# Performance work log

Hardware: AMD Instinct MI355X
Metric: run time of the kernel (lower is better)

## Reference

```python
import jax, jax.numpy as jnp
import numpy as np

B, S, D, H, F, NL, V = 4, 2048, 512, 8, 2048, 4, 32000
DH = D // H
EPS = 1e-6
LN_EPS = 1e-5


def _xavier(k, shape):
    lim = (6.0 / (shape[-2] + shape[-1])) ** 0.5
    return jax.random.uniform(k, shape, jnp.float32, -lim, lim)


def setup_inputs() -> dict:
    key = jax.random.key(0)
    ks = jax.random.split(key, 12)
    x = jax.random.randint(ks[0], (B, S), 0, V)
    emb = jax.random.normal(ks[1], (V, D), jnp.float32) * 0.02
    # sinusoidal positional encoding
    pos = np.arange(S, dtype=np.float32)[:, None]
    div = np.exp(np.arange(0, D, 2, dtype=np.float32) * (-np.log(10000.0) / D))
    pe_np = np.zeros((S, D), np.float32)
    pe_np[:, 0::2] = np.sin(pos * div)
    pe_np[:, 1::2] = np.cos(pos * div)
    pe = jnp.asarray(pe_np)
    return {
        "x": x, "emb": emb, "pe": pe,
        "Wq": _xavier(ks[2], (NL, D, D)), "bq": jnp.zeros((NL, D)),
        "Wk": _xavier(ks[3], (NL, D, D)), "bk": jnp.zeros((NL, D)),
        "Wv": _xavier(ks[4], (NL, D, D)), "bv": jnp.zeros((NL, D)),
        "Wo": _xavier(ks[5], (NL, D, D)), "bo": jnp.zeros((NL, D)),
        "W1": _xavier(ks[6], (NL, D, F)), "b1": jnp.zeros((NL, F)),
        "W2": _xavier(ks[7], (NL, F, D)), "b2": jnp.zeros((NL, D)),
        "g1": jnp.ones((NL, D)), "be1": jnp.zeros((NL, D)),
        "g2": jnp.ones((NL, D)), "be2": jnp.zeros((NL, D)),
        "gf": jnp.ones((D,)), "bf": jnp.zeros((D,)),
    }


def _layer_norm(h, g, b):
    mu = jnp.mean(h, axis=-1, keepdims=True)
    var = jnp.mean((h - mu) ** 2, axis=-1, keepdims=True)
    return (h - mu) * jax.lax.rsqrt(var + LN_EPS) * g + b


def _phi(u):
    # elu(x) + 1 feature map of fast-transformers causal-linear attention
    return jax.nn.elu(u) + 1.0


def _causal_linear_attention(q, k, v, key_mask):
    # q, k, v: [B, S, H, DH]; key_mask: [B, S] (1 for valid keys)
    Q = _phi(q)
    K = _phi(k) * key_mask[:, :, None, None]
    # cumulative state sum_{j<=i} K_j outer V_j : [B, S, H, DH, DH]
    St = jnp.cumsum(K[..., :, None] * v[..., None, :], axis=1)
    num = jnp.einsum("bshd,bshde->bshe", Q, St)
    Z = 1.0 / (jnp.einsum("bshd,bshd->bsh", Q, jnp.cumsum(K, axis=1)) + EPS)
    return num * Z[..., None]


def reference(x, emb, pe, Wq, bq, Wk, bk, Wv, bv, Wo, bo,
              W1, b1, W2, b2, g1, be1, g2, be2, gf, bf):
    # length mask from nonzero token count (LengthMask semantics)
    lengths = jnp.sum(jnp.abs(x) != 0, axis=-1)  # [B]
    key_mask = (jnp.arange(S)[None, :] < lengths[:, None]).astype(jnp.float32)
    h = emb[x] + pe[None, :, :]  # [B, S, D]
    for i in range(NL):
        q = (h @ Wq[i] + bq[i]).reshape(B, S, H, DH)
        k = (h @ Wk[i] + bk[i]).reshape(B, S, H, DH)
        v = (h @ Wv[i] + bv[i]).reshape(B, S, H, DH)
        a = _causal_linear_attention(q, k, v, key_mask).reshape(B, S, D)
        a = a @ Wo[i] + bo[i]
        h = _layer_norm(h + a, g1[i], be1[i])
        y = jax.nn.relu(h @ W1[i] + b1[i]) @ W2[i] + b2[i]
        h = _layer_norm(h + y, g2[i], be2[i])
    return _layer_norm(h, gf, bf)
```

## Files before the change

kernel.cpp:

```cpp
#include <hip/hip_runtime.h>
#include <math.h>

#define NLAYER 4
#define BB 4
#define SS 2048
#define DD 512
#define HH 8
#define DH 64
#define FF 2048
#define TT (BB*SS)
#define LCH 64
#define NCH (SS/LCH)
#define LN_EPS 1e-5f
#define ATT_EPS 1e-6f

typedef __bf16 bf16x8 __attribute__((ext_vector_type(8)));
typedef float  f32x4  __attribute__((ext_vector_type(4)));

__device__ __forceinline__ unsigned short f2bf(float f) {
    union { float f; unsigned u; } a; a.f = f;
    unsigned u = a.u;
    unsigned r = (u + 0x7FFFu + ((u >> 16) & 1u)) >> 16;
    return (unsigned short)r;
}
__device__ __forceinline__ float bf2f(unsigned short s) {
    union { unsigned u; float f; } a; a.u = ((unsigned)s) << 16;
    return a.f;
}
__device__ __forceinline__ float phi_f(float u) {
    return u > 0.f ? u + 1.f : __expf(u);
}

__global__ __launch_bounds__(64)
void len_kernel(const int* __restrict__ x, int* __restrict__ len) {
    const int b = blockIdx.x;
    int cnt = 0;
    for (int s = threadIdx.x; s < SS; s += 64) cnt += (x[b * SS + s] != 0);
    #pragma unroll
    for (int off = 32; off; off >>= 1) cnt += __shfl_xor(cnt, off);
    if (threadIdx.x == 0) len[b] = cnt;
}

__global__ __launch_bounds__(256)
void embed_kernel(const int* __restrict__ x, const float* __restrict__ emb,
                  const float* __restrict__ pe, float* __restrict__ h,
                  unsigned short* __restrict__ h_bf) {
    int t = blockIdx.x * 256 + threadIdx.x;
    int row = t >> 7;
    int q = t & 127;
    int tok = x[row];
    int s = row & (SS - 1);
    float4 e = ((const float4*)(emb + (size_t)tok * DD))[q];
    float4 p = ((const float4*)(pe + (size_t)s * DD))[q];
    float4 v; v.x = e.x + p.x; v.y = e.y + p.y; v.z = e.z + p.z; v.w = e.w + p.w;
    ((float4*)(h + (size_t)row * DD))[q] = v;
    ushort4 ub; ub.x = f2bf(v.x); ub.y = f2bf(v.y); ub.z = f2bf(v.z); ub.w = f2bf(v.w);
    ((ushort4*)(h_bf + (size_t)row * DD))[q] = ub;
}

__global__ __launch_bounds__(256)
void transpose_cvt(const float* __restrict__ src, unsigned short* __restrict__ dst,
                   int R, int C, size_t srcLS, size_t dstLS) {
    __shared__ float tile[32][33];
    const int z = blockIdx.z;
    src += (size_t)z * srcLS;
    dst += (size_t)z * dstLS;
    const int c0 = blockIdx.x * 32, r0 = blockIdx.y * 32;
    const int tx = threadIdx.x & 31, ty = threadIdx.x >> 5;
    #pragma unroll
    for (int i = 0; i < 32; i += 8)
        tile[ty + i][tx] = src[(size_t)(r0 + ty + i) * C + c0 + tx];
    __syncthreads();
    #pragma unroll
    for (int i = 0; i < 32; i += 8)
        dst[(size_t)(c0 + ty + i) * R + r0 + tx] = f2bf(tile[tx][ty + i]);
}

__global__ __launch_bounds__(256)
void bias_concat(const float* __restrict__ bq, const float* __restrict__ bk,
                 const float* __restrict__ bv, float* __restrict__ bqkv) {
    int idx = blockIdx.x * 256 + threadIdx.x;
    if (idx >= NLAYER * 1536) return;
    int l = idx / 1536, n = idx % 1536;
    float v = n < 512 ? bq[l * 512 + n] : (n < 1024 ? bk[l * 512 + n - 512] : bv[l * 512 + n - 1024]);
    bqkv[idx] = v;
}

__device__ __forceinline__ void gll16(void* lds_ptr, const void* g_ptr) {
    __builtin_amdgcn_global_load_lds(
        (const __attribute__((address_space(1))) void*)g_ptr,
        (__attribute__((address_space(3))) void*)lds_ptr, 16, 0, 0);
}

template<int RELU, int WF, int WB>
__global__ __launch_bounds__(256, 2)
void gemm_bt(const unsigned short* __restrict__ A, const unsigned short* __restrict__ Bt,
             const float* __restrict__ bias, float* __restrict__ Cf,
             unsigned short* __restrict__ Cb, int M, int N, int K) {
    __shared__ __align__(16) char lds[2 * 2 * 128 * 64 * 2];
    const int m0 = blockIdx.x * 128;
    const int n0 = blockIdx.y * 128;
    const int tid = threadIdx.x;
    const int w = tid >> 6, lane = tid & 63;
    const int wr = w >> 1, wc = w & 1;
    const int srow = lane >> 3, scc = lane & 7;

    f32x4 acc[4][4] = {};

    auto stage = [&](int buf, int k0) {
        char* base = lds + buf * 32768;
        #pragma unroll
        for (int op = 0; op < 2; ++op) {
            const unsigned short* G = op ? Bt : A;
            const int r0 = op ? n0 : m0;
            char* obase = base + op * 16384;
            #pragma unroll
            for (int i = 0; i < 4; ++i) {
                int ii = w * 4 + i;
                int row = ii * 8 + srow;
                int chunk = scc ^ (row & 7);
                gll16(obase + ii * 1024,
                      G + (size_t)(r0 + row) * K + k0 + chunk * 8);
            }
        }
    };

    stage(0, 0);
    const int nt = K >> 6;
    int buf = 0;
    const int g = lane >> 4;
    const int rA = wr * 64 + (lane & 15);
    const int rB = wc * 64 + (lane & 15);

    for (int kt = 0; kt < nt; ++kt) {
        __syncthreads();
        if (kt + 1 < nt) stage(buf ^ 1, (kt + 1) << 6);
        const char* pA = lds + buf * 32768;
        const char* pB = pA + 16384;
        bf16x8 af[4][2], bfr[4][2];
        #pragma unroll
        for (int m = 0; m < 4; ++m)
            #pragma unroll
            for (int kk = 0; kk < 2; ++kk) {
                int row = rA + m * 16;
                int c = (kk * 4 + g) ^ (row & 7);
                af[m][kk] = *(const bf16x8*)(pA + row * 128 + c * 16);
            }
        #pragma unroll
        for (int n = 0; n < 4; ++n)
            #pragma unroll
            for (int kk = 0; kk < 2; ++kk) {
                int row = rB + n * 16;
                int c = (kk * 4 + g) ^ (row & 7);
                bfr[n][kk] = *(const bf16x8*)(pB + row * 128 + c * 16);
            }
        #pragma unroll
        for (int kk = 0; kk < 2; ++kk)
            #pragma unroll
            for (int m = 0; m < 4; ++m)
                #pragma unroll
                for (int n = 0; n < 4; ++n)
                    acc[m][n] = __builtin_amdgcn_mfma_f32_16x16x32_bf16(
                        af[m][kk], bfr[n][kk], acc[m][n], 0, 0, 0);
        buf ^= 1;
    }

    const int col16 = lane & 15;
    const int rgrp = lane >> 4;
    #pragma unroll
    for (int n = 0; n < 4; ++n) {
        int col = n0 + wc * 64 + n * 16 + col16;
        float bi = bias[col];
        #pragma unroll
        for (int m = 0; m < 4; ++m) {
            int rowb = m0 + wr * 64 + m * 16 + rgrp * 4;
            #pragma unroll
            for (int r = 0; r < 4; ++r) {
                float v = acc[m][n][r] + bi;
                if (RELU) v = v > 0.f ? v : 0.f;
                if (WF) Cf[(size_t)(rowb + r) * N + col] = v;
                if (WB) Cb[(size_t)(rowb + r) * N + col] = f2bf(v);
            }
        }
    }
}

__global__ __launch_bounds__(256)
void attn_chunk_sums(const float* __restrict__ qkv, const int* __restrict__ len,
                     float* __restrict__ states, float* __restrict__ ksum) {
    const int c = blockIdx.x & (NCH - 1);
    const int bh = blockIdx.x / NCH;
    const int b = bh >> 3, h = bh & 7;
    const int L = len[b];
    const int tid = threadIdx.x;
    const int w = tid >> 6, lane = tid & 63;
    __shared__ __align__(16) unsigned short Kt[64 * 64];
    __shared__ __align__(16) unsigned short Vt[64 * 64];
    __shared__ float ksumP[4][64];

    float kpart = 0.f;
    #pragma unroll 8
    for (int t = 0; t < 16; ++t) {
        const int jj = 4 * t + w;
        const int d = lane;
        const int sglob = c * 64 + jj;
        const float* base = qkv + (size_t)(b * SS + sglob) * 1536 + h * 64 + d;
        float kv = base[512], vv = base[1024];
        float kp = (sglob < L) ? phi_f(kv) : 0.f;
        kpart += kp;
        const int sw = (((jj >> 3) ^ (d & 7)) << 3) + (jj & 7);
        Kt[d * 64 + sw] = f2bf(kp);
        Vt[d * 64 + sw] = f2bf(vv);
    }
    ksumP[w][lane] = kpart;
    __syncthreads();

    const int frow = w * 16 + (lane & 15);
    const int g = lane >> 4;
    bf16x8 ak[2];
    #pragma unroll
    for (int kk = 0; kk < 2; ++kk)
        ak[kk] = *(const bf16x8*)&Kt[frow * 64 + (((kk * 4 + g) ^ (frow & 7)) << 3)];
    f32x4 oc[4] = {};
    #pragma unroll
    for (int ef = 0; ef < 4; ++ef) {
        int brow = ef * 16 + (lane & 15);
        #pragma unroll
        for (int kk = 0; kk < 2; ++kk) {
            bf16x8 bv = *(const bf16x8*)&Vt[brow * 64 + (((kk * 4 + g) ^ (brow & 7)) << 3)];
            oc[ef] = __builtin_amdgcn_mfma_f32_16x16x32_bf16(ak[kk], bv, oc[ef], 0, 0, 0);
        }
    }
    float* so = states + (size_t)blockIdx.x * 4096;
    #pragma unroll
    for (int ef = 0; ef < 4; ++ef)
        #pragma unroll
        for (int r = 0; r < 4; ++r) {
            int dd = w * 16 + g * 4 + r;
            int e = ef * 16 + (lane & 15);
            so[dd * 64 + e] = oc[ef][r];
        }
    if (w == 0) {
        float s = ksumP[0][lane] + ksumP[1][lane] + ksumP[2][lane] + ksumP[3][lane];
        ksum[(size_t)blockIdx.x * 64 + lane] = s;
    }
}

__global__ __launch_bounds__(256)
void attn_prefix(const float* __restrict__ states, const float* __restrict__ ksum,
                 float* __restrict__ sprefix, float* __restrict__ kprefix) {
    const int bh = blockIdx.x >> 4;
    const int idx = (blockIdx.x & 15) * 256 + threadIdx.x;
    size_t base = (size_t)bh * NCH * 4096 + idx;
    float run = 0.f;
    #pragma unroll 4
    for (int cc = 0; cc < NCH; ++cc) {
        size_t o = base + (size_t)cc * 4096;
        float v = states[o];
        sprefix[o] = run;
        run += v;
    }
    if ((blockIdx.x & 15) == 0 && threadIdx.x < 64) {
        size_t kb = (size_t)bh * NCH * 64 + threadIdx.x;
        float krun = 0.f;
        for (int cc = 0; cc < NCH; ++cc) {
            size_t o = kb + (size_t)cc * 64;
            float v = ksum[o];
            kprefix[o] = krun;
            krun += v;
        }
    }
}

__global__ __launch_bounds__(256)
void attn_output(const float* __restrict__ qkv, const int* __restrict__ len,
                 const float* __restrict__ sprefix, const float* __restrict__ kprefix,
                 unsigned short* __restrict__ a_bf) {
    const int c = blockIdx.x & (NCH - 1);
    const int bh = blockIdx.x / NCH;
    const int b = bh >> 3, h = bh & 7;
    const int L = len[b];
    const int tid = threadIdx.x;
    const int w = tid >> 6, lane = tid & 63;

    __shared__ __align__(16) unsigned short Qb[64 * 64];
    __shared__ __align__(16) unsigned short Kb[64 * 64];
    __shared__ __align__(16) unsigned short SpT[64 * 64];
    __shared__ __align__(16) unsigned short Vt[64 * 64];
    __shared__ __align__(16) unsigned short Amb[64 * 64];
    __shared__ float zq[64];
    __shared__ float zinv[64];

    const float kspv = kprefix[(size_t)(bh * NCH + c) * 64 + lane];
    const float* Sp = sprefix + (size_t)(bh * NCH + c) * 4096;

    #pragma unroll 4
    for (int t = 0; t < 16; ++t) {
        const int jj = 4 * t + w;
        const int d = lane;
        const int sglob = c * 64 + jj;
        const float* base = qkv + (size_t)(b * SS + sglob) * 1536 + h * 64 + d;
        float qv = base[0], kv = base[512], vv = base[1024];
        float qp = phi_f(qv);
        float kp = (sglob < L) ? phi_f(kv) : 0.f;
        const int swr = (((d >> 3) ^ (jj & 7)) << 3) + (d & 7);
        Qb[jj * 64 + swr] = f2bf(qp);
        Kb[jj * 64 + swr] = f2bf(kp);
        const int swt = (((jj >> 3) ^ (d & 7)) << 3) + (jj & 7);
        Vt[d * 64 + swt] = f2bf(vv);
        float spv = Sp[jj * 64 + d];
        SpT[d * 64 + swt] = f2bf(spv);
        float zc = qp * kspv;
        #pragma unroll
        for (int off = 32; off; off >>= 1) zc += __shfl_xor(zc, off);
        if (lane == 0) zq[jj] = zc;
    }
    __syncthreads();

    const int frow = w * 16 + (lane & 15);
    const int g = lane >> 4;
    bf16x8 aq[2];
    #pragma unroll
    for (int kk = 0; kk < 2; ++kk)
        aq[kk] = *(const bf16x8*)&Qb[frow * 64 + (((kk * 4 + g) ^ (frow & 7)) << 3)];

    f32x4 am[4] = {};
    #pragma unroll
    for (int jf = 0; jf < 4; ++jf) {
        int brow = jf * 16 + (lane & 15);
        #pragma unroll
        for (int kk = 0; kk < 2; ++kk) {
            bf16x8 bk = *(const bf16x8*)&Kb[brow * 64 + (((kk * 4 + g) ^ (brow & 7)) << 3)];
            am[jf] = __builtin_amdgcn_mfma_f32_16x16x32_bf16(aq[kk], bk, am[jf], 0, 0, 0);
        }
    }

    float zl[4] = {0.f, 0.f, 0.f, 0.f};
    #pragma unroll
    for (int jf = 0; jf < 4; ++jf) {
        #pragma unroll
        for (int r = 0; r < 4; ++r) {
            int i = w * 16 + g * 4 + r;
            int j = jf * 16 + (lane & 15);
            float v = (j <= i) ? am[jf][r] : 0.f;
            zl[r] += v;
            Amb[i * 64 + (((j >> 3) ^ (i & 7)) << 3) + (j & 7)] = f2bf(v);
        }
    }
    #pragma unroll
    for (int r = 0; r < 4; ++r)
        #pragma unroll
        for (int off = 1; off < 16; off <<= 1) zl[r] += __shfl_xor(zl[r], off);
    #pragma unroll
    for (int r = 0; r < 4; ++r) {
        if ((lane & 15) == r) {
            int i = w * 16 + g * 4 + r;
            zinv[i] = 1.f / (zl[r] + zq[i] + ATT_EPS);
        }
    }

    f32x4 oc[4] = {};
    #pragma unroll
    for (int ef = 0; ef < 4; ++ef) {
        int brow = ef * 16 + (lane & 15);
        #pragma unroll
        for (int kk = 0; kk < 2; ++kk) {
            bf16x8 bs = *(const bf16x8*)&SpT[brow * 64 + (((kk * 4 + g) ^ (brow & 7)) << 3)];
            oc[ef] = __builtin_amdgcn_mfma_f32_16x16x32_bf16(aq[kk], bs, oc[ef], 0, 0, 0);
        }
    }
    bf16x8 aam[2];
    #pragma unroll
    for (int kk = 0; kk < 2; ++kk)
        aam[kk] = *(const bf16x8*)&Amb[frow * 64 + (((kk * 4 + g) ^ (frow & 7)) << 3)];
    #pragma unroll
    for (int ef = 0; ef < 4; ++ef) {
        int brow = ef * 16 + (lane & 15);
        #pragma unroll
        for (int kk = 0; kk < 2; ++kk) {
            bf16x8 bv = *(const bf16x8*)&Vt[brow * 64 + (((kk * 4 + g) ^ (brow & 7)) << 3)];
            oc[ef] = __builtin_amdgcn_mfma_f32_16x16x32_bf16(aam[kk], bv, oc[ef], 0, 0, 0);
        }
    }

    __syncthreads();
    #pragma unroll
    for (int ef = 0; ef < 4; ++ef) {
        #pragma unroll
        for (int r = 0; r < 4; ++r) {
            int i = w * 16 + g * 4 + r;
            int e = ef * 16 + (lane & 15);
            float zi = zinv[i];
            Kb[i * 64 + (((e >> 3) ^ (i & 7)) << 3) + (e & 7)] = f2bf(oc[ef][r] * zi);
        }
    }
    __syncthreads();
    {
        unsigned short* dst = a_bf + (size_t)(b * SS + c * 64) * 512 + h * 64;
        #pragma unroll
        for (int u = 0; u < 2; ++u) {
            int cid = tid + u * 256;
            int row = cid >> 3, cb = cid & 7;
            int4 val = *(const int4*)&Kb[row * 64 + ((cb ^ (row & 7)) << 3)];
            *(int4*)(dst + (size_t)row * 512 + cb * 8) = val;
        }
    }
}

template<int ADD, int WB>
__global__ __launch_bounds__(64)
void ln_kernel(const float* __restrict__ hin, const float* __restrict__ add,
               const float* __restrict__ gw, const float* __restrict__ bw,
               float* __restrict__ hout, unsigned short* __restrict__ hbf) {
    const int row = blockIdx.x;
    const int lane = threadIdx.x;
    float v[8];
    const float* hp = hin + (size_t)row * DD;
    float s = 0.f;
    #pragma unroll
    for (int i = 0; i < 2; ++i) {
        int q = lane + i * 64;
        float4 a = ((const float4*)hp)[q];
        if (ADD) {
            float4 bb = ((const float4*)(add + (size_t)row * DD))[q];
            a.x += bb.x; a.y += bb.y; a.z += bb.z; a.w += bb.w;
        }
        v[i*4+0] = a.x; v[i*4+1] = a.y; v[i*4+2] = a.z; v[i*4+3] = a.w;
        s += a.x + a.y + a.z + a.w;
    }
    #pragma unroll
    for (int off = 32; off; off >>= 1) s += __shfl_xor(s, off);
    float mu = s * (1.f / 512.f);
    float sq = 0.f;
    #pragma unroll
    for (int i = 0; i < 8; ++i) { float d = v[i] - mu; sq += d * d; }
    #pragma unroll
    for (int off = 32; off; off >>= 1) sq += __shfl_xor(sq, off);
    float rs = 1.f / sqrtf(sq * (1.f / 512.f) + LN_EPS);
    #pragma unroll
    for (int i = 0; i < 2; ++i) {
        int q = lane + i * 64;
        float4 gv = ((const float4*)gw)[q];
        float4 bv = ((const float4*)bw)[q];
        float4 o;
        o.x = (v[i*4+0] - mu) * rs * gv.x + bv.x;
        o.y = (v[i*4+1] - mu) * rs * gv.y + bv.y;
        o.z = (v[i*4+2] - mu) * rs * gv.z + bv.z;
        o.w = (v[i*4+3] - mu) * rs * gv.w + bv.w;
        ((float4*)(hout + (size_t)row * DD))[q] = o;
        if (WB) {
            ushort4 ub; ub.x = f2bf(o.x); ub.y = f2bf(o.y); ub.z = f2bf(o.z); ub.w = f2bf(o.w);
            ((ushort4*)(hbf + (size_t)row * DD))[q] = ub;
        }
    }
}

extern "C" void kernel_launch(void* const* d_in, const int* in_sizes, int n_in,
                              void* d_out, int out_size, void* d_ws, size_t ws_size,
                              hipStream_t stream) {
    (void)in_sizes; (void)n_in; (void)out_size; (void)ws_size;
    const int*   x   = (const int*)d_in[0];
    const float* emb = (const float*)d_in[1];
    const float* pe  = (const float*)d_in[2];
    const float* Wq  = (const float*)d_in[3];
    const float* bq  = (const float*)d_in[4];
    const float* Wk  = (const float*)d_in[5];
    const float* bk  = (const float*)d_in[6];
    const float* Wv  = (const float*)d_in[7];
    const float* bv  = (const float*)d_in[8];
    const float* Wo  = (const float*)d_in[9];
    const float* bo  = (const float*)d_in[10];
    const float* W1  = (const float*)d_in[11];
    const float* b1  = (const float*)d_in[12];
    const float* W2  = (const float*)d_in[13];
    const float* b2  = (const float*)d_in[14];
    const float* g1  = (const float*)d_in[15];
    const float* be1 = (const float*)d_in[16];
    const float* g2  = (const float*)d_in[17];
    const float* be2 = (const float*)d_in[18];
    const float* gf  = (const float*)d_in[19];
    const float* bff = (const float*)d_in[20];
    float* out = (float*)d_out;

    char* ws = (char*)d_ws;
    size_t off = 0;
    auto alloc = [&](size_t bytes) -> void* {
        void* p = ws + off; off += (bytes + 255) & ~(size_t)255; return p;
    };
    int* len              = (int*)alloc(16);
    unsigned short* qkv_t = (unsigned short*)alloc((size_t)NLAYER * 1536 * 512 * 2);
    unsigned short* wo_t  = (unsigned short*)alloc((size_t)NLAYER * 512 * 512 * 2);
    unsigned short* w1_t  = (unsigned short*)alloc((size_t)NLAYER * 2048 * 512 * 2);
    unsigned short* w2_t  = (unsigned short*)alloc((size_t)NLAYER * 512 * 2048 * 2);
    float* bqkv           = (float*)alloc((size_t)NLAYER * 1536 * 4);
    float* h              = (float*)alloc((size_t)TT * 512 * 4);
    unsigned short* h_bf  = (unsigned short*)alloc((size_t)TT * 512 * 2);
    float* qkv            = (float*)alloc((size_t)TT * 1536 * 4);
    unsigned short* a_bf  = (unsigned short*)alloc((size_t)TT * 512 * 2);
    float* obuf           = (float*)alloc((size_t)TT * 512 * 4);
    unsigned short* y1_bf = (unsigned short*)alloc((size_t)TT * 2048 * 2);
    float* states         = (float*)alloc((size_t)32 * NCH * 4096 * 4);
    float* ksum           = (float*)alloc((size_t)32 * NCH * 64 * 4);
    float* sprefix        = (float*)alloc((size_t)32 * NCH * 4096 * 4);
    float* kprefix        = (float*)alloc((size_t)32 * NCH * 64 * 4);

    len_kernel<<<BB, 64, 0, stream>>>(x, len);
    embed_kernel<<<(TT * 128) / 256, 256, 0, stream>>>(x, emb, pe, h, h_bf);

    dim3 tb(256);
    transpose_cvt<<<dim3(16, 16, NLAYER), tb, 0, stream>>>(Wq, qkv_t,             512, 512, (size_t)512*512, (size_t)1536*512);
    transpose_cvt<<<dim3(16, 16, NLAYER), tb, 0, stream>>>(Wk, qkv_t + 512*512,   512, 512, (size_t)512*512, (size_t)1536*512);
    transpose_cvt<<<dim3(16, 16, NLAYER), tb, 0, stream>>>(Wv, qkv_t + 1024*512,  512, 512, (size_t)512*512, (size_t)1536*512);
    transpose_cvt<<<dim3(16, 16, NLAYER), tb, 0, stream>>>(Wo, wo_t,              512, 512, (size_t)512*512, (size_t)512*512);
    transpose_cvt<<<dim3(64, 16, NLAYER), tb, 0, stream>>>(W1, w1_t,              512, 2048, (size_t)512*2048, (size_t)2048*512);
    transpose_cvt<<<dim3(16, 64, NLAYER), tb, 0, stream>>>(W2, w2_t,              2048, 512, (size_t)2048*512, (size_t)512*2048);
    bias_concat<<<(NLAYER * 1536 + 255) / 256, 256, 0, stream>>>(bq, bk, bv, bqkv);

    for (int l = 0; l < NLAYER; ++l) {
        gemm_bt<0,1,0><<<dim3(TT/128, 1536/128), 256, 0, stream>>>(
            h_bf, qkv_t + (size_t)l*1536*512, bqkv + l*1536, qkv, nullptr, TT, 1536, 512);
        attn_chunk_sums<<<32 * NCH, 256, 0, stream>>>(qkv, len, states, ksum);
        attn_prefix<<<32 * 16, 256, 0, stream>>>(states, ksum, sprefix, kprefix);
        attn_output<<<32 * NCH, 256, 0, stream>>>(qkv, len, sprefix, kprefix, a_bf);
        gemm_bt<0,1,0><<<dim3(TT/128, 512/128), 256, 0, stream>>>(
            a_bf, wo_t + (size_t)l*512*512, bo + l*512, obuf, nullptr, TT, 512, 512);
        ln_kernel<1,1><<<TT, 64, 0, stream>>>(h, obuf, g1 + l*512, be1 + l*512, h, h_bf);
        gemm_bt<1,0,1><<<dim3(TT/128, 2048/128), 256, 0, stream>>>(
            h_bf, w1_t + (size_t)l*2048*512, b1 + l*2048, nullptr, y1_bf, TT, 2048, 512);
        gemm_bt<0,1,0><<<dim3(TT/128, 512/128), 256, 0, stream>>>(
            y1_bf, w2_t + (size_t)l*512*2048, b2 + l*512, obuf, nullptr, TT, 512, 2048);
        ln_kernel<1,1><<<TT, 64, 0, stream>>>(h, obuf, g2 + l*512, be2 + l*512, h, h_bf);
    }
    ln_kernel<0,0><<<TT, 64, 0, stream>>>(h, nullptr, gf, bff, out, nullptr);
}
```

Before: 648.9 us.

## Store QKV and attention chunk states in bf16 and swizzle GEMM block order

The QKV projection now writes bf16 instead of fp32. The attention kernels read those bf16 values directly, and the per-chunk states and prefix states are stored in bf16, which cuts global memory traffic for the attention stages. The GEMM grid is flattened to 1D and block indices are remapped in an XCD-style swizzle so that neighbouring tiles land on the same die for L2 reuse. The trade-off is lower precision: q and k are rounded to bf16 before the feature map, and the chunk states are rounded before the prefix accumulation.

Result: faster. 594.5 us (-8.4%).

```diff
diff --git a/kernel.cpp b/kernel.cpp
--- a/kernel.cpp
+++ b/kernel.cpp
@@ -98,8 +98,11 @@
              const float* __restrict__ bias, float* __restrict__ Cf,
              unsigned short* __restrict__ Cb, int M, int N, int K) {
     __shared__ __align__(16) char lds[2 * 2 * 128 * 64 * 2];
-    const int m0 = blockIdx.x * 128;
-    const int n0 = blockIdx.y * 128;
+    const int Nt = N >> 7;
+    const int bid = blockIdx.x;
+    const int swz = (bid & 7) * ((int)gridDim.x >> 3) + (bid >> 3);
+    const int m0 = (swz / Nt) * 128;
+    const int n0 = (swz % Nt) * 128;
     const int tid = threadIdx.x;
     const int w = tid >> 6, lane = tid & 63;
     const int wr = w >> 1, wc = w & 1;
@@ -186,8 +189,8 @@
 }
 
 __global__ __launch_bounds__(256)
-void attn_chunk_sums(const float* __restrict__ qkv, const int* __restrict__ len,
-                     float* __restrict__ states, float* __restrict__ ksum) {
+void attn_chunk_sums(const unsigned short* __restrict__ qkv, const int* __restrict__ len,
+                     unsigned short* __restrict__ states, float* __restrict__ ksum) {
     const int c = blockIdx.x & (NCH - 1);
     const int bh = blockIdx.x / NCH;
     const int b = bh >> 3, h = bh & 7;
@@ -204,13 +207,13 @@
         const int jj = 4 * t + w;
         const int d = lane;
         const int sglob = c * 64 + jj;
-        const float* base = qkv + (size_t)(b * SS + sglob) * 1536 + h * 64 + d;
-        float kv = base[512], vv = base[1024];
+        const unsigned short* base = qkv + (size_t)(b * SS + sglob) * 1536 + h * 64 + d;
+        float kv = bf2f(base[512]);
         float kp = (sglob < L) ? phi_f(kv) : 0.f;
         kpart += kp;
         const int sw = (((jj >> 3) ^ (d & 7)) << 3) + (jj & 7);
         Kt[d * 64 + sw] = f2bf(kp);
-        Vt[d * 64 + sw] = f2bf(vv);
+        Vt[d * 64 + sw] = base[1024];
     }
     ksumP[w][lane] = kpart;
     __syncthreads();
@@ -231,14 +234,14 @@
             oc[ef] = __builtin_amdgcn_mfma_f32_16x16x32_bf16(ak[kk], bv, oc[ef], 0, 0, 0);
         }
     }
-    float* so = states + (size_t)blockIdx.x * 4096;
+    unsigned short* so = states + (size_t)blockIdx.x * 4096;
     #pragma unroll
     for (int ef = 0; ef < 4; ++ef)
         #pragma unroll
         for (int r = 0; r < 4; ++r) {
             int dd = w * 16 + g * 4 + r;
             int e = ef * 16 + (lane & 15);
-            so[dd * 64 + e] = oc[ef][r];
+            so[dd * 64 + e] = f2bf(oc[ef][r]);
         }
     if (w == 0) {
         float s = ksumP[0][lane] + ksumP[1][lane] + ksumP[2][lane] + ksumP[3][lane];
@@ -247,8 +250,8 @@
 }
 
 __global__ __launch_bounds__(256)
-void attn_prefix(const float* __restrict__ states, const float* __restrict__ ksum,
-                 float* __restrict__ sprefix, float* __restrict__ kprefix) {
+void attn_prefix(const unsigned short* __restrict__ states, const float* __restrict__ ksum,
+                 unsigned short* __restrict__ sprefix, float* __restrict__ kprefix) {
     const int bh = blockIdx.x >> 4;
     const int idx = (blockIdx.x & 15) * 256 + threadIdx.x;
     size_t base = (size_t)bh * NCH * 4096 + idx;
@@ -256,8 +259,8 @@
     #pragma unroll 4
     for (int cc = 0; cc < NCH; ++cc) {
         size_t o = base + (size_t)cc * 4096;
-        float v = states[o];
-        sprefix[o] = run;
+        float v = bf2f(states[o]);
+        sprefix[o] = f2bf(run);
         run += v;
     }
     if ((blockIdx.x & 15) == 0 && threadIdx.x < 64) {
@@ -273,8 +276,8 @@
 }
 
 __global__ __launch_bounds__(256)
-void attn_output(const float* __restrict__ qkv, const int* __restrict__ len,
-                 const float* __restrict__ sprefix, const float* __restrict__ kprefix,
+void attn_output(const unsigned short* __restrict__ qkv, const int* __restrict__ len,
+                 const unsigned short* __restrict__ sprefix, const float* __restrict__ kprefix,
                  unsigned short* __restrict__ a_bf) {
     const int c = blockIdx.x & (NCH - 1);
     const int bh = blockIdx.x / NCH;
@@ -292,24 +295,23 @@
     __shared__ float zinv[64];
 
     const float kspv = kprefix[(size_t)(bh * NCH + c) * 64 + lane];
-    const float* Sp = sprefix + (size_t)(bh * NCH + c) * 4096;
+    const unsigned short* Sp = sprefix + (size_t)(bh * NCH + c) * 4096;
 
     #pragma unroll 4
     for (int t = 0; t < 16; ++t) {
         const int jj = 4 * t + w;
         const int d = lane;
         const int sglob = c * 64 + jj;
-        const float* base = qkv + (size_t)(b * SS + sglob) * 1536 + h * 64 + d;
-        float qv = base[0], kv = base[512], vv = base[1024];
+        const unsigned short* base = qkv + (size_t)(b * SS + sglob) * 1536 + h * 64 + d;
+        float qv = bf2f(base[0]), kv = bf2f(base[512]);
         float qp = phi_f(qv);
         float kp = (sglob < L) ? phi_f(kv) : 0.f;
         const int swr = (((d >> 3) ^ (jj & 7)) << 3) + (d & 7);
         Qb[jj * 64 + swr] = f2bf(qp);
         Kb[jj * 64 + swr] = f2bf(kp);
         const int swt = (((jj >> 3) ^ (d & 7)) << 3) + (jj & 7);
-        Vt[d * 64 + swt] = f2bf(vv);
-        float spv = Sp[jj * 64 + d];
-        SpT[d * 64 + swt] = f2bf(spv);
+        Vt[d * 64 + swt] = base[1024];
+        SpT[d * 64 + swt] = Sp[jj * 64 + d];
         float zc = qp * kspv;
         #pragma unroll
         for (int off = 32; off; off >>= 1) zc += __shfl_xor(zc, off);
@@ -495,13 +497,13 @@
     float* bqkv           = (float*)alloc((size_t)NLAYER * 1536 * 4);
     float* h              = (float*)alloc((size_t)TT * 512 * 4);
     unsigned short* h_bf  = (unsigned short*)alloc((size_t)TT * 512 * 2);
-    float* qkv            = (float*)alloc((size_t)TT * 1536 * 4);
+    unsigned short* qkv   = (unsigned short*)alloc((size_t)TT * 1536 * 2);
     unsigned short* a_bf  = (unsigned short*)alloc((size_t)TT * 512 * 2);
     float* obuf           = (float*)alloc((size_t)TT * 512 * 4);
     unsigned short* y1_bf = (unsigned short*)alloc((size_t)TT * 2048 * 2);
-    float* states         = (float*)alloc((size_t)32 * NCH * 4096 * 4);
+    unsigned short* states  = (unsigned short*)alloc((size_t)32 * NCH * 4096 * 2);
     float* ksum           = (float*)alloc((size_t)32 * NCH * 64 * 4);
-    float* sprefix        = (float*)alloc((size_t)32 * NCH * 4096 * 4);
+    unsigned short* sprefix = (unsigned short*)alloc((size_t)32 * NCH * 4096 * 2);
     float* kprefix        = (float*)alloc((size_t)32 * NCH * 64 * 4);
 
     len_kernel<<<BB, 64, 0, stream>>>(x, len);
@@ -517,17 +519,17 @@
     bias_concat<<<(NLAYER * 1536 + 255) / 256, 256, 0, stream>>>(bq, bk, bv, bqkv);
 
     for (int l = 0; l < NLAYER; ++l) {
-        gemm_bt<0,1,0><<<dim3(TT/128, 1536/128), 256, 0, stream>>>(
-            h_bf, qkv_t + (size_t)l*1536*512, bqkv + l*1536, qkv, nullptr, TT, 1536, 512);
+        gemm_bt<0,0,1><<<(TT/128) * (1536/128), 256, 0, stream>>>(
+            h_bf, qkv_t + (size_t)l*1536*512, bqkv + l*1536, nullptr, qkv, TT, 1536, 512);
         attn_chunk_sums<<<32 * NCH, 256, 0, stream>>>(qkv, len, states, ksum);
         attn_prefix<<<32 * 16, 256, 0, stream>>>(states, ksum, sprefix, kprefix);
         attn_output<<<32 * NCH, 256, 0, stream>>>(qkv, len, sprefix, kprefix, a_bf);
-        gemm_bt<0,1,0><<<dim3(TT/128, 512/128), 256, 0, stream>>>(
+        gemm_bt<0,1,0><<<(TT/128) * (512/128), 256, 0, stream>>>(
             a_bf, wo_t + (size_t)l*512*512, bo + l*512, obuf, nullptr, TT, 512, 512);
         ln_kernel<1,1><<<TT, 64, 0, stream>>>(h, obuf, g1 + l*512, be1 + l*512, h, h_bf);
-        gemm_bt<1,0,1><<<dim3(TT/128, 2048/128), 256, 0, stream>>>(
+        gemm_bt<1,0,1><<<(TT/128) * (2048/128), 256, 0, stream>>>(
             h_bf, w1_t + (size_t)l*2048*512, b1 + l*2048, nullptr, y1_bf, TT, 2048, 512);
-        gemm_bt<0,1,0><<<dim3(TT/128, 512/128), 256, 0, stream>>>(
+        gemm_bt<0,1,0><<<(TT/128) * (512/128), 256, 0, stream>>>(
             y1_bf, w2_t + (size_t)l*512*2048, b2 + l*512, obuf, nullptr, TT, 512, 2048);
         ln_kernel<1,1><<<TT, 64, 0, stream>>>(h, obuf, g2 + l*512, be2 + l*512, h, h_bf);
     }
```
